# Kernel tuning notes

Measured on AMD Instinct MI355X. Metric: run time of the kernel, lower is better.

Reference implementation:

```python
import jax, jax.numpy as jnp
import numpy as np

B, S, D, H = 4, 2048, 1024, 16
HD = D // H  # head dim = 64


def setup_inputs() -> dict:
    key = jax.random.key(0)
    ks = jax.random.split(key, 9)
    scale = 1.0 / np.sqrt(D)
    return {
        "x": jax.random.normal(ks[0], (B, S, D), dtype=jnp.float32),
        "Wq": jax.random.normal(ks[1], (D, D), dtype=jnp.float32) * scale,
        "bq": jnp.zeros((D,), dtype=jnp.float32),
        "Wk": jax.random.normal(ks[2], (D, D), dtype=jnp.float32) * scale,
        "bk": jnp.zeros((D,), dtype=jnp.float32),
        "Wv": jax.random.normal(ks[3], (D, D), dtype=jnp.float32) * scale,
        "bv": jnp.zeros((D,), dtype=jnp.float32),
        "Wo": jax.random.normal(ks[4], (D, D), dtype=jnp.float32) * scale,
        "bo": jnp.zeros((D,), dtype=jnp.float32),
    }


def _split_heads(t):
    # [B,S,D] -> [B,H,S,HD]
    return t.reshape(t.shape[0], t.shape[1], H, HD).transpose(0, 2, 1, 3)


def reference(x, Wq, bq, Wk, bk, Wv, bv, Wo, bo):
    q = _split_heads(x @ Wq + bq)
    k = _split_heads(x @ Wk + bk)
    v = _split_heads(x @ Wv + bv)
    # scaled dot-product attention; scale by sqrt of key dim (= head dim)
    scores = jnp.einsum("bhqd,bhkd->bhqk", q, k) / jnp.sqrt(jnp.asarray(HD, q.dtype))
    weights = jax.nn.softmax(scores, axis=-1)
    attn = jnp.einsum("bhqk,bhkd->bhqd", weights, v)
    concat = attn.transpose(0, 2, 1, 3).reshape(x.shape[0], -1, D)
    out = concat @ Wo + bo
    return out, weights
```

## Files before the change

kernel.cpp:

```cpp
#include <hip/hip_runtime.h>
#include <cstddef>
#include <cstdint>

static constexpr int BB = 4;
static constexpr int SS = 2048;
static constexpr int DD = 1024;
static constexpr int HH = 16;
static constexpr int HDIM = 64;
static constexpr int MROWS = BB * SS;

typedef __attribute__((ext_vector_type(4))) float f32x4;
typedef __bf16 bf16x8 __attribute__((ext_vector_type(8)));
typedef __bf16 bf16x4 __attribute__((ext_vector_type(4)));

#define GLB_U32(p) ((const __attribute__((address_space(1))) uint32_t*)(p))
#define LDS_U32(p) ((__attribute__((address_space(3))) uint32_t*)(p))

__device__ __forceinline__ float fexp2(float x) {
#if __has_builtin(__builtin_amdgcn_exp2f)
    return __builtin_amdgcn_exp2f(x);
#else
    return exp2f(x);
#endif
}

__global__ __launch_bounds__(256) void cvt_x(const float* __restrict__ x,
                                             __bf16* __restrict__ xb)
{
    size_t i = ((size_t)blockIdx.x * 256 + threadIdx.x) * 8;
    float4 a = *reinterpret_cast<const float4*>(x + i);
    float4 b = *reinterpret_cast<const float4*>(x + i + 4);
    bf16x8 v;
    v[0] = (__bf16)a.x; v[1] = (__bf16)a.y; v[2] = (__bf16)a.z; v[3] = (__bf16)a.w;
    v[4] = (__bf16)b.x; v[5] = (__bf16)b.y; v[6] = (__bf16)b.z; v[7] = (__bf16)b.w;
    *reinterpret_cast<bf16x8*>(xb + i) = v;
}

__global__ __launch_bounds__(256) void transpose_w(
    const float* __restrict__ W0, const float* __restrict__ W1,
    const float* __restrict__ W2, const float* __restrict__ W3,
    __bf16* __restrict__ wt_base)
{
    const float* W = (blockIdx.z == 0) ? W0 : (blockIdx.z == 1) ? W1
                   : (blockIdx.z == 2) ? W2 : W3;
    __bf16* WT = wt_base + (size_t)blockIdx.z * 1048576;

    __shared__ float T[64][68];
    const int t = threadIdx.x;
    const int n0 = blockIdx.x * 64, k0 = blockIdx.y * 64;

#pragma unroll
    for (int it = 0; it < 4; ++it) {
        const int row = it * 16 + (t >> 4);
        const int col = (t & 15) * 4;
        float4 v = *reinterpret_cast<const float4*>(&W[(size_t)(k0 + row) * 1024 + n0 + col]);
        T[row][col + 0] = v.x; T[row][col + 1] = v.y;
        T[row][col + 2] = v.z; T[row][col + 3] = v.w;
    }
    __syncthreads();

#pragma unroll
    for (int it = 0; it < 2; ++it) {
        const int idx = it * 256 + t;
        const int n = idx >> 3, ch = idx & 7;
        bf16x8 v;
#pragma unroll
        for (int e = 0; e < 8; ++e) v[e] = (__bf16)T[ch * 8 + e][n];
        *reinterpret_cast<bf16x8*>(&WT[(size_t)(n0 + n) * 1024 + k0 + ch * 8]) = v;
    }
}

template <int MODE>
__global__ __launch_bounds__(256) void gemm_bf16(
    const __bf16* __restrict__ A,
    const __bf16* __restrict__ BT,
    const float* __restrict__ bias,
    void* __restrict__ Cout)
{
    __shared__ __bf16 At[128 * 32];
    __shared__ __bf16 Bt[128 * 32];

    constexpr float OSC = (MODE == 0) ? 0.18033688011112042f : 1.0f;

    const int t = threadIdx.x;
    const int w = t >> 6, l = t & 63, l16 = l & 15, lg = l >> 4;
    const int m0 = blockIdx.x * 128, n0 = blockIdx.y * 128;
    const int wr = w >> 1, wc = w & 1;

    f32x4 acc[4][4] = {};

    for (int k0 = 0; k0 < 1024; k0 += 32) {
#pragma unroll
        for (int r = 0; r < 2; ++r) {
            const int cb = (w * 2 + r) * 64;
            const int ch = cb + l;
            const __bf16* srcA = A + (size_t)(m0 + (ch >> 2)) * 1024 + k0 + (ch & 3) * 8;
            __builtin_amdgcn_global_load_lds(GLB_U32(srcA), LDS_U32(At + cb * 8), 16, 0, 0);
        }
#pragma unroll
        for (int r = 0; r < 2; ++r) {
            const int cb = (w * 2 + r) * 64;
            const int ch = cb + l;
            const __bf16* srcB = BT + (size_t)(n0 + (ch >> 2)) * 1024 + k0 + (ch & 3) * 8;
            __builtin_amdgcn_global_load_lds(GLB_U32(srcB), LDS_U32(Bt + cb * 8), 16, 0, 0);
        }
        __syncthreads();

        bf16x8 af[4], bf[4];
#pragma unroll
        for (int i = 0; i < 4; ++i) {
            af[i] = *reinterpret_cast<const bf16x8*>(At + (wr * 64 + i * 16 + l16) * 32 + lg * 8);
            bf[i] = *reinterpret_cast<const bf16x8*>(Bt + (wc * 64 + i * 16 + l16) * 32 + lg * 8);
        }
#pragma unroll
        for (int i = 0; i < 4; ++i)
#pragma unroll
            for (int j = 0; j < 4; ++j)
                acc[i][j] = __builtin_amdgcn_mfma_f32_16x16x32_bf16(af[i], bf[j], acc[i][j], 0, 0, 0);
        __syncthreads();
    }

    if constexpr (MODE == 2) {
        __shared__ __bf16 Tr[4][64][72];
#pragma unroll
        for (int i = 0; i < 4; ++i)
#pragma unroll
            for (int j = 0; j < 4; ++j)
#pragma unroll
                for (int r = 0; r < 4; ++r) {
                    const int n = n0 + wc * 64 + j * 16 + l16;
                    Tr[w][j * 16 + l16][i * 16 + lg * 4 + r] =
                        (__bf16)(acc[i][j][r] + bias[n]);
                }
        asm volatile("s_waitcnt lgkmcnt(0)" ::: "memory");
        __bf16* V = (__bf16*)Cout;
#pragma unroll
        for (int it = 0; it < 8; ++it) {
            const int idx = it * 64 + l;
            const int np = idx >> 3, c = idx & 7;
            bf16x8 v = *reinterpret_cast<const bf16x8*>(&Tr[w][np][c * 8]);
            const int gn = n0 + wc * 64 + np;
            const int m  = m0 + wr * 64 + c * 8;
            const size_t o = (((size_t)(m >> 11) * HH + (gn >> 6)) * HDIM + (gn & 63)) * SS + (m & 2047);
            *reinterpret_cast<bf16x8*>(V + o) = v;
        }
    } else {
#pragma unroll
        for (int i = 0; i < 4; ++i)
#pragma unroll
            for (int j = 0; j < 4; ++j) {
                const int n = n0 + wc * 64 + j * 16 + l16;
                const float bv = bias[n];
#pragma unroll
                for (int r = 0; r < 4; ++r) {
                    const int m = m0 + wr * 64 + i * 16 + lg * 4 + r;
                    const float v = (acc[i][j][r] + bv) * OSC;
                    if constexpr (MODE == 3) {
                        ((float*)Cout)[(size_t)m * 1024 + n] = v;
                    } else {
                        const size_t o = (((size_t)(m >> 11) * HH + (n >> 6)) * SS + (m & 2047)) * HDIM + (n & 63);
                        ((__bf16*)Cout)[o] = (__bf16)v;
                    }
                }
            }
    }
}

__device__ __forceinline__ void stage64x64(const __bf16* __restrict__ g, int rstride,
                                           __bf16* lds, int t)
{
#pragma unroll
    for (int it = 0; it < 2; ++it) {
        const int i = it * 256 + t;
        const int r = i >> 3, j = i & 7;
        const __bf16* src = g + (size_t)r * rstride + ((j ^ (r & 7)) << 3);
        __builtin_amdgcn_global_load_lds(GLB_U32(src), LDS_U32(lds + i * 8), 16, 0, 0);
    }
}

__device__ __forceinline__ bf16x8 ldsF(const __bf16* buf, int row, int c0)
{
    return *(const bf16x8*)(buf + row * 64 + (((c0 >> 3) ^ (row & 7)) << 3));
}

__global__ __launch_bounds__(256) void attn_fused(
    const __bf16* __restrict__ Qg, const __bf16* __restrict__ Kg,
    const __bf16* __restrict__ VTg, float* __restrict__ Wout,
    __bf16* __restrict__ attnb)
{
    __shared__ __bf16 Ksh[2][64 * 64];
    __shared__ __bf16 Vsh[2][64 * 64];
    __shared__ __bf16 Psh[4][16 * 64];

    const int t = threadIdx.x, w = t >> 6, l = t & 63, l16 = l & 15, lg = l >> 4;

    int bid = (int)blockIdx.x;
    bid = (bid & 7) * 256 + (bid >> 3);
    const int qt = bid & 31, bh = bid >> 5;
    const int qr = qt * 64 + w * 16;

    const __bf16* Qp = Qg + ((size_t)bh * SS + qr) * HDIM;
    const __bf16* Kp = Kg + (size_t)bh * SS * HDIM;
    const __bf16* Vp = VTg + (size_t)bh * HDIM * SS;

    const bf16x8 aq0 = *(const bf16x8*)(Qp + l16 * 64 + lg * 8);
    const bf16x8 aq1 = *(const bf16x8*)(Qp + l16 * 64 + 32 + lg * 8);

    char* pbase = (char*)&Psh[w][0];

    float ssum = 0.f;
    f32x4 o[4] = {};

    stage64x64(Kp, 64, Ksh[0], t);
    stage64x64(Vp, SS, Vsh[0], t);
    __syncthreads();

    for (int kt = 0; kt < 32; ++kt) {
        if (kt < 31) {
            stage64x64(Kp + (kt + 1) * 4096, 64, Ksh[(kt + 1) & 1], t);
            stage64x64(Vp + (kt + 1) * 64, SS, Vsh[(kt + 1) & 1], t);
        }
        const __bf16* kb = Ksh[kt & 1];
        const __bf16* vb = Vsh[kt & 1];

#pragma unroll
        for (int c4 = 0; c4 < 4; ++c4) {
            const bf16x8 b0 = ldsF(kb, c4 * 16 + l16, lg * 8);
            const bf16x8 b1 = ldsF(kb, c4 * 16 + l16, 32 + lg * 8);
            f32x4 a = {0.f, 0.f, 0.f, 0.f};
            a = __builtin_amdgcn_mfma_f32_16x16x32_bf16(b0, aq0, a, 0, 0, 0);
            a = __builtin_amdgcn_mfma_f32_16x16x32_bf16(b1, aq1, a, 0, 0, 0);
            float p0 = fexp2(a[0]), p1 = fexp2(a[1]), p2 = fexp2(a[2]), p3 = fexp2(a[3]);
            ssum += (p0 + p1) + (p2 + p3);
            bf16x4 pk;
            pk[0] = (__bf16)p0; pk[1] = (__bf16)p1; pk[2] = (__bf16)p2; pk[3] = (__bf16)p3;
            const int off = l16 * 128 + ((c4 * 32 + lg * 8) ^ ((l16 & 7) << 4));
            *(bf16x4*)(pbase + off) = pk;
        }
        asm volatile("s_waitcnt lgkmcnt(0)" ::: "memory");
        __builtin_amdgcn_sched_barrier(0);

        bf16x8 pa[2];
#pragma unroll
        for (int kc = 0; kc < 2; ++kc) {
            const int off = l16 * 128 + ((kc * 64 + lg * 16) ^ ((l16 & 7) << 4));
            pa[kc] = *(const bf16x8*)(pbase + off);
        }
#pragma unroll
        for (int nt = 0; nt < 4; ++nt) {
            const bf16x8 bv0 = ldsF(vb, nt * 16 + l16, lg * 8);
            const bf16x8 bv1 = ldsF(vb, nt * 16 + l16, 32 + lg * 8);
            o[nt] = __builtin_amdgcn_mfma_f32_16x16x32_bf16(pa[0], bv0, o[nt], 0, 0, 0);
            o[nt] = __builtin_amdgcn_mfma_f32_16x16x32_bf16(pa[1], bv1, o[nt], 0, 0, 0);
        }
        __syncthreads();
    }

    stage64x64(Kp, 64, Ksh[0], t);

    ssum += __shfl_xor(ssum, 16);
    ssum += __shfl_xor(ssum, 32);
    const float linv = 1.0f / ssum;

    float os[4];
#pragma unroll
    for (int r = 0; r < 4; ++r) os[r] = __shfl(linv, lg * 4 + r);

    const int b = bh >> 4, h = bh & 15;
#pragma unroll
    for (int nt = 0; nt < 4; ++nt)
#pragma unroll
        for (int r = 0; r < 4; ++r) {
            const int srow = qr + lg * 4 + r;
            attnb[((size_t)b * SS + srow) * DD + h * 64 + nt * 16 + l16] =
                (__bf16)(o[nt][r] * os[r]);
        }
    __syncthreads();

    float* wbase = Wout + ((size_t)bh * SS + qr + l16) * SS;

    for (int kt = 0; kt < 32; ++kt) {
        if (kt < 31) stage64x64(Kp + (kt + 1) * 4096, 64, Ksh[(kt + 1) & 1], t);
        const __bf16* kb = Ksh[kt & 1];

#pragma unroll
        for (int c4 = 0; c4 < 4; ++c4) {
            const bf16x8 b0 = ldsF(kb, c4 * 16 + l16, lg * 8);
            const bf16x8 b1 = ldsF(kb, c4 * 16 + l16, 32 + lg * 8);
            f32x4 a = {0.f, 0.f, 0.f, 0.f};
            a = __builtin_amdgcn_mfma_f32_16x16x32_bf16(b0, aq0, a, 0, 0, 0);
            a = __builtin_amdgcn_mfma_f32_16x16x32_bf16(b1, aq1, a, 0, 0, 0);
            f32x4 pv;
            pv[0] = fexp2(a[0]) * linv; pv[1] = fexp2(a[1]) * linv;
            pv[2] = fexp2(a[2]) * linv; pv[3] = fexp2(a[3]) * linv;
            __builtin_nontemporal_store(pv,
                (f32x4*)(wbase + kt * 64 + c4 * 16 + lg * 4));
        }
        __syncthreads();
    }
}

extern "C" void kernel_launch(void* const* d_in, const int* in_sizes, int n_in,
                              void* d_out, int out_size, void* d_ws, size_t ws_size,
                              hipStream_t stream)
{
    const float* x  = (const float*)d_in[0];
    const float* Wq = (const float*)d_in[1];
    const float* bq = (const float*)d_in[2];
    const float* Wk = (const float*)d_in[3];
    const float* bk = (const float*)d_in[4];
    const float* Wv = (const float*)d_in[5];
    const float* bv = (const float*)d_in[6];
    const float* Wo = (const float*)d_in[7];
    const float* bo = (const float*)d_in[8];

    float* out     = (float*)d_out;
    float* weights = out + (size_t)BB * SS * DD;

    __bf16* ws = (__bf16*)d_ws;
    const size_t NX = (size_t)MROWS * DD;
    __bf16* xb    = ws;
    __bf16* wtb   = xb + NX;
    __bf16* wqT   = wtb;
    __bf16* wkT   = wtb + 1048576;
    __bf16* wvT   = wtb + 2097152;
    __bf16* woT   = wtb + 3145728;
    __bf16* qb    = wtb + 4194304;
    __bf16* kb    = qb + NX;
    __bf16* vtb   = kb + NX;
    __bf16* attnb = vtb + NX;

    dim3 blk(256);

    cvt_x<<<dim3(4096), blk, 0, stream>>>(x, xb);
    transpose_w<<<dim3(16, 16, 4), blk, 0, stream>>>(Wq, Wk, Wv, Wo, wtb);

    dim3 ggrid(MROWS / 128, DD / 128);
    gemm_bf16<0><<<ggrid, blk, 0, stream>>>(xb, wqT, bq, qb);
    gemm_bf16<1><<<ggrid, blk, 0, stream>>>(xb, wkT, bk, kb);
    gemm_bf16<2><<<ggrid, blk, 0, stream>>>(xb, wvT, bv, vtb);

    attn_fused<<<dim3(2048), blk, 0, stream>>>(qb, kb, vtb, weights, attnb);

    gemm_bf16<3><<<ggrid, blk, 0, stream>>>(attnb, woT, bo, out);
}
```

Baseline: 465.2 us.

## Process two query tiles per block, fusing tile B's PV pass into tile A's write pass

Each block now handles two 64-row query tiles instead of one and launches half as many blocks. Tile A's probability-write sweep is merged with tile B's sum-and-PV sweep, so one staged K tile feeds both, and K/V are streamed three times per two tiles instead of four. Launch bounds now request 4 blocks per CU. The cost is more live registers (two Q fragments and two accumulator sets) and a longer serial chain per block with half the grid parallelism.

```diff
diff --git a/kernel.cpp b/kernel.cpp
--- a/kernel.cpp
+++ b/kernel.cpp
@@ -183,7 +183,7 @@
     return *(const bf16x8*)(buf + row * 64 + (((c0 >> 3) ^ (row & 7)) << 3));
 }
 
-__global__ __launch_bounds__(256) void attn_fused(
+__global__ __launch_bounds__(256, 4) void attn_fused(
     const __bf16* __restrict__ Qg, const __bf16* __restrict__ Kg,
     const __bf16* __restrict__ VTg, float* __restrict__ Wout,
     __bf16* __restrict__ attnb)
@@ -195,21 +195,26 @@
     const int t = threadIdx.x, w = t >> 6, l = t & 63, l16 = l & 15, lg = l >> 4;
 
     int bid = (int)blockIdx.x;
-    bid = (bid & 7) * 256 + (bid >> 3);
-    const int qt = bid & 31, bh = bid >> 5;
-    const int qr = qt * 64 + w * 16;
-
-    const __bf16* Qp = Qg + ((size_t)bh * SS + qr) * HDIM;
+    bid = (bid & 7) * 128 + (bid >> 3);
+    const int qp = bid & 15, bh = bid >> 4;
+    const int qrA = qp * 128 + w * 16;
+    const int qrB = qrA + 64;
+
     const __bf16* Kp = Kg + (size_t)bh * SS * HDIM;
     const __bf16* Vp = VTg + (size_t)bh * HDIM * SS;
-
-    const bf16x8 aq0 = *(const bf16x8*)(Qp + l16 * 64 + lg * 8);
-    const bf16x8 aq1 = *(const bf16x8*)(Qp + l16 * 64 + 32 + lg * 8);
+    const __bf16* QpA = Qg + ((size_t)bh * SS + qrA) * HDIM;
+    const __bf16* QpB = Qg + ((size_t)bh * SS + qrB) * HDIM;
+
+    const bf16x8 aqA0 = *(const bf16x8*)(QpA + l16 * 64 + lg * 8);
+    const bf16x8 aqA1 = *(const bf16x8*)(QpA + l16 * 64 + 32 + lg * 8);
+    const bf16x8 aqB0 = *(const bf16x8*)(QpB + l16 * 64 + lg * 8);
+    const bf16x8 aqB1 = *(const bf16x8*)(QpB + l16 * 64 + 32 + lg * 8);
 
     char* pbase = (char*)&Psh[w][0];
-
-    float ssum = 0.f;
-    f32x4 o[4] = {};
+    const int b = bh >> 4, h = bh & 15;
+
+    float ssumA = 0.f, ssumB = 0.f;
+    f32x4 oA[4] = {}, oB[4] = {};
 
     stage64x64(Kp, 64, Ksh[0], t);
     stage64x64(Vp, SS, Vsh[0], t);
@@ -228,10 +233,10 @@
             const bf16x8 b0 = ldsF(kb, c4 * 16 + l16, lg * 8);
             const bf16x8 b1 = ldsF(kb, c4 * 16 + l16, 32 + lg * 8);
             f32x4 a = {0.f, 0.f, 0.f, 0.f};
-            a = __builtin_amdgcn_mfma_f32_16x16x32_bf16(b0, aq0, a, 0, 0, 0);
-            a = __builtin_amdgcn_mfma_f32_16x16x32_bf16(b1, aq1, a, 0, 0, 0);
+            a = __builtin_amdgcn_mfma_f32_16x16x32_bf16(b0, aqA0, a, 0, 0, 0);
+            a = __builtin_amdgcn_mfma_f32_16x16x32_bf16(b1, aqA1, a, 0, 0, 0);
             float p0 = fexp2(a[0]), p1 = fexp2(a[1]), p2 = fexp2(a[2]), p3 = fexp2(a[3]);
-            ssum += (p0 + p1) + (p2 + p3);
+            ssumA += (p0 + p1) + (p2 + p3);
             bf16x4 pk;
             pk[0] = (__bf16)p0; pk[1] = (__bf16)p1; pk[2] = (__bf16)p2; pk[3] = (__bf16)p3;
             const int off = l16 * 128 + ((c4 * 32 + lg * 8) ^ ((l16 & 7) << 4));
@@ -250,51 +255,123 @@
         for (int nt = 0; nt < 4; ++nt) {
             const bf16x8 bv0 = ldsF(vb, nt * 16 + l16, lg * 8);
             const bf16x8 bv1 = ldsF(vb, nt * 16 + l16, 32 + lg * 8);
-            o[nt] = __builtin_amdgcn_mfma_f32_16x16x32_bf16(pa[0], bv0, o[nt], 0, 0, 0);
-            o[nt] = __builtin_amdgcn_mfma_f32_16x16x32_bf16(pa[1], bv1, o[nt], 0, 0, 0);
+            oA[nt] = __builtin_amdgcn_mfma_f32_16x16x32_bf16(pa[0], bv0, oA[nt], 0, 0, 0);
+            oA[nt] = __builtin_amdgcn_mfma_f32_16x16x32_bf16(pa[1], bv1, oA[nt], 0, 0, 0);
         }
         __syncthreads();
     }
 
     stage64x64(Kp, 64, Ksh[0], t);
-
-    ssum += __shfl_xor(ssum, 16);
-    ssum += __shfl_xor(ssum, 32);
-    const float linv = 1.0f / ssum;
-
-    float os[4];
-#pragma unroll
-    for (int r = 0; r < 4; ++r) os[r] = __shfl(linv, lg * 4 + r);
-
-    const int b = bh >> 4, h = bh & 15;
-#pragma unroll
-    for (int nt = 0; nt < 4; ++nt)
-#pragma unroll
-        for (int r = 0; r < 4; ++r) {
-            const int srow = qr + lg * 4 + r;
-            attnb[((size_t)b * SS + srow) * DD + h * 64 + nt * 16 + l16] =
-                (__bf16)(o[nt][r] * os[r]);
-        }
+    stage64x64(Vp, SS, Vsh[0], t);
+
+    ssumA += __shfl_xor(ssumA, 16);
+    ssumA += __shfl_xor(ssumA, 32);
+    const float linvA = 1.0f / ssumA;
+    {
+        float os[4];
+#pragma unroll
+        for (int r = 0; r < 4; ++r) os[r] = __shfl(linvA, lg * 4 + r);
+#pragma unroll
+        for (int nt = 0; nt < 4; ++nt)
+#pragma unroll
+            for (int r = 0; r < 4; ++r) {
+                const int srow = qrA + lg * 4 + r;
+                attnb[((size_t)b * SS + srow) * DD + h * 64 + nt * 16 + l16] =
+                    (__bf16)(oA[nt][r] * os[r]);
+            }
+    }
     __syncthreads();
 
-    float* wbase = Wout + ((size_t)bh * SS + qr + l16) * SS;
+    float* wbaseA = Wout + ((size_t)bh * SS + qrA + l16) * SS;
 
     for (int kt = 0; kt < 32; ++kt) {
-        if (kt < 31) stage64x64(Kp + (kt + 1) * 4096, 64, Ksh[(kt + 1) & 1], t);
+        if (kt < 31) {
+            stage64x64(Kp + (kt + 1) * 4096, 64, Ksh[(kt + 1) & 1], t);
+            stage64x64(Vp + (kt + 1) * 64, SS, Vsh[(kt + 1) & 1], t);
+        }
         const __bf16* kb = Ksh[kt & 1];
+        const __bf16* vb = Vsh[kt & 1];
 
 #pragma unroll
         for (int c4 = 0; c4 < 4; ++c4) {
             const bf16x8 b0 = ldsF(kb, c4 * 16 + l16, lg * 8);
             const bf16x8 b1 = ldsF(kb, c4 * 16 + l16, 32 + lg * 8);
             f32x4 a = {0.f, 0.f, 0.f, 0.f};
-            a = __builtin_amdgcn_mfma_f32_16x16x32_bf16(b0, aq0, a, 0, 0, 0);
-            a = __builtin_amdgcn_mfma_f32_16x16x32_bf16(b1, aq1, a, 0, 0, 0);
+            a = __builtin_amdgcn_mfma_f32_16x16x32_bf16(b0, aqA0, a, 0, 0, 0);
+            a = __builtin_amdgcn_mfma_f32_16x16x32_bf16(b1, aqA1, a, 0, 0, 0);
+            f32x4 pvA;
+            pvA[0] = fexp2(a[0]) * linvA; pvA[1] = fexp2(a[1]) * linvA;
+            pvA[2] = fexp2(a[2]) * linvA; pvA[3] = fexp2(a[3]) * linvA;
+            __builtin_nontemporal_store(pvA,
+                (f32x4*)(wbaseA + kt * 64 + c4 * 16 + lg * 4));
+            f32x4 bacc = {0.f, 0.f, 0.f, 0.f};
+            bacc = __builtin_amdgcn_mfma_f32_16x16x32_bf16(b0, aqB0, bacc, 0, 0, 0);
+            bacc = __builtin_amdgcn_mfma_f32_16x16x32_bf16(b1, aqB1, bacc, 0, 0, 0);
+            float p0 = fexp2(bacc[0]), p1 = fexp2(bacc[1]),
+                  p2 = fexp2(bacc[2]), p3 = fexp2(bacc[3]);
+            ssumB += (p0 + p1) + (p2 + p3);
+            bf16x4 pk;
+            pk[0] = (__bf16)p0; pk[1] = (__bf16)p1; pk[2] = (__bf16)p2; pk[3] = (__bf16)p3;
+            const int off = l16 * 128 + ((c4 * 32 + lg * 8) ^ ((l16 & 7) << 4));
+            *(bf16x4*)(pbase + off) = pk;
+        }
+        asm volatile("s_waitcnt lgkmcnt(0)" ::: "memory");
+        __builtin_amdgcn_sched_barrier(0);
+
+        bf16x8 pa[2];
+#pragma unroll
+        for (int kc = 0; kc < 2; ++kc) {
+            const int off = l16 * 128 + ((kc * 64 + lg * 16) ^ ((l16 & 7) << 4));
+            pa[kc] = *(const bf16x8*)(pbase + off);
+        }
+#pragma unroll
+        for (int nt = 0; nt < 4; ++nt) {
+            const bf16x8 bv0 = ldsF(vb, nt * 16 + l16, lg * 8);
+            const bf16x8 bv1 = ldsF(vb, nt * 16 + l16, 32 + lg * 8);
+            oB[nt] = __builtin_amdgcn_mfma_f32_16x16x32_bf16(pa[0], bv0, oB[nt], 0, 0, 0);
+            oB[nt] = __builtin_amdgcn_mfma_f32_16x16x32_bf16(pa[1], bv1, oB[nt], 0, 0, 0);
+        }
+        __syncthreads();
+    }
+
+    stage64x64(Kp, 64, Ksh[0], t);
+
+    ssumB += __shfl_xor(ssumB, 16);
+    ssumB += __shfl_xor(ssumB, 32);
+    const float linvB = 1.0f / ssumB;
+    {
+        float os[4];
+#pragma unroll
+        for (int r = 0; r < 4; ++r) os[r] = __shfl(linvB, lg * 4 + r);
+#pragma unroll
+        for (int nt = 0; nt < 4; ++nt)
+#pragma unroll
+            for (int r = 0; r < 4; ++r) {
+                const int srow = qrB + lg * 4 + r;
+                attnb[((size_t)b * SS + srow) * DD + h * 64 + nt * 16 + l16] =
+                    (__bf16)(oB[nt][r] * os[r]);
+            }
+    }
+    __syncthreads();
+
+    float* wbaseB = Wout + ((size_t)bh * SS + qrB + l16) * SS;
+
+    for (int kt = 0; kt < 32; ++kt) {
+        if (kt < 31) stage64x64(Kp + (kt + 1) * 4096, 64, Ksh[(kt + 1) & 1], t);
+        const __bf16* kb = Ksh[kt & 1];
+
+#pragma unroll
+        for (int c4 = 0; c4 < 4; ++c4) {
+            const bf16x8 b0 = ldsF(kb, c4 * 16 + l16, lg * 8);
+            const bf16x8 b1 = ldsF(kb, c4 * 16 + l16, 32 + lg * 8);
+            f32x4 a = {0.f, 0.f, 0.f, 0.f};
+            a = __builtin_amdgcn_mfma_f32_16x16x32_bf16(b0, aqB0, a, 0, 0, 0);
+            a = __builtin_amdgcn_mfma_f32_16x16x32_bf16(b1, aqB1, a, 0, 0, 0);
             f32x4 pv;
-            pv[0] = fexp2(a[0]) * linv; pv[1] = fexp2(a[1]) * linv;
-            pv[2] = fexp2(a[2]) * linv; pv[3] = fexp2(a[3]) * linv;
+            pv[0] = fexp2(a[0]) * linvB; pv[1] = fexp2(a[1]) * linvB;
+            pv[2] = fexp2(a[2]) * linvB; pv[3] = fexp2(a[3]) * linvB;
             __builtin_nontemporal_store(pv,
-                (f32x4*)(wbase + kt * 64 + c4 * 16 + lg * 4));
+                (f32x4*)(wbaseB + kt * 64 + c4 * 16 + lg * 4));
         }
         __syncthreads();
     }
@@ -340,7 +417,7 @@
     gemm_bf16<1><<<ggrid, blk, 0, stream>>>(xb, wkT, bk, kb);
     gemm_bf16<2><<<ggrid, blk, 0, stream>>>(xb, wvT, bv, vtb);
 
-    attn_fused<<<dim3(2048), blk, 0, stream>>>(qb, kb, vtb, weights, attnb);
+    attn_fused<<<dim3(1024), blk, 0, stream>>>(qb, kb, vtb, weights, attnb);
 
     gemm_bf16<3><<<ggrid, blk, 0, stream>>>(attnb, woT, bo, out);
 }
```

After: 500.0 us. 7.5% more time.
